# Performance work log

Hardware: AMD Instinct MI355X
Metric: run time of the kernel (lower is better)

Reference implementation:

```python
import jax, jax.numpy as jnp
import numpy as np

B, C, H, W = 256, 3, 224, 224
IMG_SIZE = 224
BRIGHT, CONTRAST, SAT, HUE = 0.2, 0.2, 0.2, 0.05
P_JITTER, P_CROP = 0.8, 0.5
SCALE_MIN, SCALE_MAX = 0.85, 1.0


def _blend(a, b, ratio):
    # torchvision _blend with float bound 1.0
    return jnp.clip(ratio * a + (1.0 - ratio) * b, 0.0, 1.0)


def _grayscale(x):
    # x: [B,3,H,W] -> [B,H,W]
    return 0.299 * x[:, 0] + 0.587 * x[:, 1] + 0.114 * x[:, 2]


def _adjust_hue(x, hue):
    # x: [B,3,H,W], hue: [B,1,1] offset in [-0.5,0.5]
    r, g, b = x[:, 0], x[:, 1], x[:, 2]
    maxc = jnp.maximum(jnp.maximum(r, g), b)
    minc = jnp.minimum(jnp.minimum(r, g), b)
    v = maxc
    cr = maxc - minc
    eqc = cr == 0.0
    s = cr / jnp.where(eqc, 1.0, maxc)
    crd = jnp.where(eqc, 1.0, cr)
    rc = (maxc - r) / crd
    gc = (maxc - g) / crd
    bc = (maxc - b) / crd
    h = ((maxc == r) * (bc - gc)
         + ((maxc == g) & (maxc != r)) * (2.0 + rc - bc)
         + ((maxc != g) & (maxc != r)) * (4.0 + gc - rc))
    h = jnp.mod(h / 6.0 + 1.0, 1.0)
    h = jnp.mod(h + hue, 1.0)
    # hsv -> rgb
    h6 = h * 6.0
    i = jnp.floor(h6)
    f = h6 - i
    i = i.astype(jnp.int32) % 6
    p = v * (1.0 - s)
    q = v * (1.0 - s * f)
    t = v * (1.0 - s * (1.0 - f))
    m = [(i == k) for k in range(6)]
    r2 = m[0] * v + m[1] * q + m[2] * p + m[3] * p + m[4] * t + m[5] * v
    g2 = m[0] * t + m[1] * v + m[2] * v + m[3] * q + m[4] * p + m[5] * p
    b2 = m[0] * p + m[1] * p + m[2] * t + m[3] * v + m[4] * v + m[5] * q
    return jnp.stack([r2, g2, b2], axis=1)


def _crop_resize_one(im, top, left, ch, cw):
    # im: [C,H,W]; bilinear resize of crop box to IMG_SIZE x IMG_SIZE
    Hh, Ww = im.shape[1], im.shape[2]
    S = IMG_SIZE
    ys = jnp.clip(top + (jnp.arange(S) + 0.5) * ch / S - 0.5, 0.0, Hh - 1.0)
    xs = jnp.clip(left + (jnp.arange(S) + 0.5) * cw / S - 0.5, 0.0, Ww - 1.0)
    y0 = jnp.floor(ys); x0 = jnp.floor(xs)
    wy = (ys - y0)[None, :, None]  # [1,S,1]
    wx = (xs - x0)[None, None, :]  # [1,1,S]
    y0i = y0.astype(jnp.int32); y1i = jnp.minimum(y0i + 1, Hh - 1)
    x0i = x0.astype(jnp.int32); x1i = jnp.minimum(x0i + 1, Ww - 1)
    g = lambda yi, xi: im[:, yi[:, None], xi[None, :]]  # [C,S,S]
    row0 = (1.0 - wx) * g(y0i, x0i) + wx * g(y0i, x1i)
    row1 = (1.0 - wx) * g(y1i, x0i) + wx * g(y1i, x1i)
    return (1.0 - wy) * row0 + wy * row1


def _forward(img, u_jitter, u_bright, u_contrast, u_sat, u_hue, u_crop, u_scale, u_top, u_left):
    # --- color jitter (fixed op order: brightness, contrast, saturation, hue) ---
    bf = (1.0 + (2.0 * u_bright - 1.0) * BRIGHT)[:, None, None, None]
    cf = (1.0 + (2.0 * u_contrast - 1.0) * CONTRAST)[:, None, None, None]
    sf = (1.0 + (2.0 * u_sat - 1.0) * SAT)[:, None, None, None]
    hf = ((2.0 * u_hue - 1.0) * HUE)[:, None, None]
    x = _blend(img, jnp.zeros_like(img), bf)                      # brightness
    mean_gray = _grayscale(x).mean(axis=(-2, -1))[:, None, None, None]
    x = _blend(x, mean_gray, cf)                                  # contrast
    x = _blend(x, _grayscale(x)[:, None], sf)                     # saturation
    x = _adjust_hue(x, hf)                                        # hue
    x = jnp.clip(x, 0.0, 1.0)
    jitter_on = (u_jitter < P_JITTER)[:, None, None, None]
    img = jnp.where(jitter_on, x, img)
    # --- random crop + resize back to IMG_SIZE ---
    Hh, Ww = img.shape[2], img.shape[3]
    scale = SCALE_MIN + (SCALE_MAX - SCALE_MIN) * u_scale
    ch = jnp.floor(Hh * scale)
    cw = jnp.floor(Ww * scale)
    top = jnp.clip(jnp.floor(u_top * (Hh - ch + 1.0)), 0.0, Hh - ch)
    left = jnp.clip(jnp.floor(u_left * (Ww - cw + 1.0)), 0.0, Ww - cw)
    resized = jax.vmap(_crop_resize_one)(img, top, left, ch, cw)
    crop_on = (u_crop < P_CROP)[:, None, None, None]
    return jnp.where(crop_on, resized, img)


def setup_inputs() -> dict:
    key = jax.random.key(0)
    ks = jax.random.split(key, 10)
    names = ['u_jitter', 'u_bright', 'u_contrast', 'u_sat', 'u_hue',
             'u_crop', 'u_scale', 'u_top', 'u_left']
    inp = {'img': jax.random.uniform(ks[0], (B, C, H, W), dtype=jnp.float32)}
    for i, n in enumerate(names):
        inp[n] = jax.random.uniform(ks[i + 1], (B,), dtype=jnp.float32)
    return inp


def reference(img, u_jitter, u_bright, u_contrast, u_sat, u_hue, u_crop, u_scale, u_top, u_left):
    return _forward(img, u_jitter, u_bright, u_contrast, u_sat, u_hue,
                    u_crop, u_scale, u_top, u_left)
```

## Files before the change

### kernel.cpp

```cpp
#include <hip/hip_runtime.h>


static constexpr int   kB      = 256;
static constexpr int   kHW     = 224;
static constexpr int   kHW4    = kHW / 4;
static constexpr int   kNPix   = kHW * kHW;
static constexpr int   kPlane  = kNPix;
static constexpr int   kPlane4 = kNPix / 4;
static constexpr int   kRows   = 8;
static constexpr int   kSrcRows = kRows + 1;
static constexpr int   kParts  = 8;
static constexpr int   kQuadsPerPart = kPlane4 / kParts;

__device__ __forceinline__ float clamp01(float x) {
    return fminf(fmaxf(x, 0.0f), 1.0f);
}

__device__ __forceinline__ float fast_rcp(float x) {
#if __has_builtin(__builtin_amdgcn_rcpf)
    return __builtin_amdgcn_rcpf(x);
#else
    return 1.0f / x;
#endif
}

struct Px { float r, g, b; };

__device__ __forceinline__ Px jitter_px(Px p, float bf, float cf, float sf,
                                        float hf, float oc) {
    float r = clamp01(bf * p.r);
    float g = clamp01(bf * p.g);
    float b = clamp01(bf * p.b);
    r = clamp01(cf * r + oc);
    g = clamp01(cf * g + oc);
    b = clamp01(cf * b + oc);
    float gray = 0.299f * r + 0.587f * g + 0.114f * b;
    float os = (1.0f - sf) * gray;
    r = clamp01(sf * r + os);
    g = clamp01(sf * g + os);
    b = clamp01(sf * b + os);
    float maxc = fmaxf(fmaxf(r, g), b);
    float minc = fminf(fminf(r, g), b);
    float v  = maxc;
    float cr = maxc - minc;
    bool  eqc = (cr == 0.0f);
    float s   = eqc ? 0.0f : cr * fast_rcp(maxc);
    float inv = eqc ? 1.0f : fast_rcp(cr);
    float rc = (maxc - r) * inv;
    float gc = (maxc - g) * inv;
    float bc = (maxc - b) * inv;
    float h = (maxc == r) ? (bc - gc)
            : (maxc == g) ? (2.0f + rc - bc)
                          : (4.0f + gc - rc);
    h = h * 0.16666667f + 1.0f;
    h = h - floorf(h);
    h = h + hf;
    h = h - floorf(h);
    float h6 = h * 6.0f;
    float fi = floorf(h6);
    float f  = h6 - fi;
    int   i  = ((int)fi) % 6;
    float pp = v * (1.0f - s);
    float qq = v * (1.0f - s * f);
    float tt = v * (1.0f - s * (1.0f - f));
    float r2 = (i == 1) ? qq : ((i == 2) || (i == 3)) ? pp : (i == 4) ? tt : v;
    float g2 = (i == 0) ? tt : ((i == 1) || (i == 2)) ? v  : (i == 3) ? qq : pp;
    float b2 = ((i == 0) || (i == 1)) ? pp : (i == 2) ? tt : (i == 5) ? qq : v;
    Px o;
    o.r = clamp01(r2);
    o.g = clamp01(g2);
    o.b = clamp01(b2);
    return o;
}

__device__ __forceinline__ void jitter_quad(float4& r4, float4& g4, float4& b4,
                                            float bf, float cf, float sf,
                                            float hf, float oc) {
    Px a0 = jitter_px({r4.x, g4.x, b4.x}, bf, cf, sf, hf, oc);
    Px a1 = jitter_px({r4.y, g4.y, b4.y}, bf, cf, sf, hf, oc);
    Px a2 = jitter_px({r4.z, g4.z, b4.z}, bf, cf, sf, hf, oc);
    Px a3 = jitter_px({r4.w, g4.w, b4.w}, bf, cf, sf, hf, oc);
    r4 = {a0.r, a1.r, a2.r, a3.r};
    g4 = {a0.g, a1.g, a2.g, a3.g};
    b4 = {a0.b, a1.b, a2.b, a3.b};
}

__global__ __launch_bounds__(256)
void gray_mean_kernel(const float* __restrict__ img,
                      const float* __restrict__ u_jitter,
                      const float* __restrict__ u_bright,
                      float* __restrict__ gray_part)
{
    const int b    = blockIdx.y;
    const int part = blockIdx.x;
    if (u_jitter[b] >= 0.8f) return;
    const float bf = 1.0f + (2.0f * u_bright[b] - 1.0f) * 0.2f;
    const float4* pr = (const float4*)(img + (size_t)b * 3 * kPlane)
                     + part * kQuadsPerPart;
    const float4* pg = pr + kPlane4;
    const float4* pb = pr + 2 * kPlane4;
    float acc = 0.0f;
    for (int i = threadIdx.x; i < kQuadsPerPart; i += 256) {
        float4 r = pr[i], g = pg[i], bl = pb[i];
        acc += 0.299f * clamp01(bf * r.x) + 0.587f * clamp01(bf * g.x) + 0.114f * clamp01(bf * bl.x);
        acc += 0.299f * clamp01(bf * r.y) + 0.587f * clamp01(bf * g.y) + 0.114f * clamp01(bf * bl.y);
        acc += 0.299f * clamp01(bf * r.z) + 0.587f * clamp01(bf * g.z) + 0.114f * clamp01(bf * bl.z);
        acc += 0.299f * clamp01(bf * r.w) + 0.587f * clamp01(bf * g.w) + 0.114f * clamp01(bf * bl.w);
    }
#pragma unroll
    for (int off = 32; off > 0; off >>= 1)
        acc += __shfl_down(acc, off);
    __shared__ float red[4];
    const int lane = threadIdx.x & 63;
    const int w    = threadIdx.x >> 6;
    if (lane == 0) red[w] = acc;
    __syncthreads();
    if (threadIdx.x == 0)
        gray_part[b * kParts + part] = red[0] + red[1] + red[2] + red[3];
}

__global__ __launch_bounds__(256)
void aug_main_kernel(const float* __restrict__ img,
                     const float* __restrict__ u_jitter,
                     const float* __restrict__ u_bright,
                     const float* __restrict__ u_contrast,
                     const float* __restrict__ u_sat,
                     const float* __restrict__ u_hue,
                     const float* __restrict__ u_crop,
                     const float* __restrict__ u_scale,
                     const float* __restrict__ u_top,
                     const float* __restrict__ u_left,
                     const float* __restrict__ gray_part,
                     float* __restrict__ out)
{
    const int b   = blockIdx.y;
    const int oy0 = blockIdx.x * kRows;
    const int t   = threadIdx.x;

    const bool jitter_on = u_jitter[b] < 0.8f;
    const bool crop_on   = u_crop[b]   < 0.5f;

    float bf = 1.0f, cf = 1.0f, sf = 1.0f, hf = 0.0f, oc = 0.0f;
    if (jitter_on) {
        bf = 1.0f + (2.0f * u_bright[b]   - 1.0f) * 0.2f;
        cf = 1.0f + (2.0f * u_contrast[b] - 1.0f) * 0.2f;
        sf = 1.0f + (2.0f * u_sat[b]      - 1.0f) * 0.2f;
        hf = (2.0f * u_hue[b] - 1.0f) * 0.05f;
        float s = 0.0f;
#pragma unroll
        for (int k = 0; k < kParts; ++k) s += gray_part[b * kParts + k];
        const float mg = s * (1.0f / (float)kNPix);
        oc = (1.0f - cf) * mg;
    }

    const float*  base  = img + (size_t)b * 3 * kPlane;
    float*        obase = out + (size_t)b * 3 * kPlane;
    const float4* p4    = (const float4*)base;
    float4*       o4    = (float4*)obase;

    if (!crop_on) {
        for (int q = t; q < kRows * kHW4; q += 256) {
            const int f4 = oy0 * kHW4 + q;
            float4 r4 = p4[f4];
            float4 g4 = p4[f4 + kPlane4];
            float4 b4 = p4[f4 + 2 * kPlane4];
            if (jitter_on) jitter_quad(r4, g4, b4, bf, cf, sf, hf, oc);
            o4[f4]               = r4;
            o4[f4 + kPlane4]     = g4;
            o4[f4 + 2 * kPlane4] = b4;
        }
        return;
    }

    float ch, top, left;
    {
#pragma clang fp contract(off)
        float scale = 0.85f + 0.15f * u_scale[b];
        ch = floorf(224.0f * scale);
        float rem = (224.0f - ch) + 1.0f;
        top  = fminf(fmaxf(floorf(u_top[b]  * rem), 0.0f), 224.0f - ch);
        left = fminf(fmaxf(floorf(u_left[b] * rem), 0.0f), 224.0f - ch);
    }

    int ybase;
    {
#pragma clang fp contract(off)
        float fy0 = top + ((float)oy0 + 0.5f) * ch / 224.0f - 0.5f;
        fy0 = fminf(fmaxf(fy0, 0.0f), 223.0f);
        ybase = (int)floorf(fy0);
    }
    ybase = min(ybase, kHW - kSrcRows);

    __shared__ float sm[3][kSrcRows * kHW];

    for (int q = t; q < kSrcRows * kHW4; q += 256) {
        const int r  = q / kHW4;
        const int xq = q - r * kHW4;
        const int gi = (ybase + r) * kHW4 + xq;
        float4 r4 = p4[gi];
        float4 g4 = p4[gi + kPlane4];
        float4 b4 = p4[gi + 2 * kPlane4];
        if (jitter_on) jitter_quad(r4, g4, b4, bf, cf, sf, hf, oc);
        const int so = r * kHW + xq * 4;
        *(float4*)&sm[0][so] = r4;
        *(float4*)&sm[1][so] = g4;
        *(float4*)&sm[2][so] = b4;
    }
    __syncthreads();

    for (int p = t; p < kRows * kHW; p += 256) {
        const int dy = p / kHW;
        const int ox = p - dy * kHW;
        const int oy = oy0 + dy;
        float fy;
        {
#pragma clang fp contract(off)
            fy = top + ((float)oy + 0.5f) * ch / 224.0f - 0.5f;
        }
        fy = fminf(fmaxf(fy, 0.0f), 223.0f);
        const float y0f = floorf(fy);
        const float wy  = fy - y0f;
        const int   y0  = (int)y0f;
        const int   y1  = min(y0 + 1, kHW - 1);
        const int   r0  = (y0 - ybase) * kHW;
        const int   r1  = (y1 - ybase) * kHW;

        float fx;
        {
#pragma clang fp contract(off)
            fx = left + ((float)ox + 0.5f) * ch / 224.0f - 0.5f;
        }
        fx = fminf(fmaxf(fx, 0.0f), 223.0f);
        const float x0f = floorf(fx);
        const float wx  = fx - x0f;
        const int   x0  = (int)x0f;
        const int   x1  = min(x0 + 1, kHW - 1);

        const int oo = oy * kHW + ox;
#pragma unroll
        for (int c = 0; c < 3; ++c) {
            const float v00 = sm[c][r0 + x0];
            const float v01 = sm[c][r0 + x1];
            const float v10 = sm[c][r1 + x0];
            const float v11 = sm[c][r1 + x1];
            const float a0 = (1.0f - wx) * v00 + wx * v01;
            const float a1 = (1.0f - wx) * v10 + wx * v11;
            obase[c * kPlane + oo] = (1.0f - wy) * a0 + wy * a1;
        }
    }
}

extern "C" void kernel_launch(void* const* d_in, const int* in_sizes, int n_in,
                              void* d_out, int out_size, void* d_ws, size_t ws_size,
                              hipStream_t stream) {
    const float* img = (const float*)d_in[0];
    const float* uj  = (const float*)d_in[1];
    const float* ub  = (const float*)d_in[2];
    const float* uc  = (const float*)d_in[3];
    const float* us  = (const float*)d_in[4];
    const float* uh  = (const float*)d_in[5];
    const float* ucr = (const float*)d_in[6];
    const float* usc = (const float*)d_in[7];
    const float* ut  = (const float*)d_in[8];
    const float* ul  = (const float*)d_in[9];
    float* gray_part = (float*)d_ws;
    float* out       = (float*)d_out;

    gray_mean_kernel<<<dim3(kParts, kB), 256, 0, stream>>>(img, uj, ub, gray_part);

    dim3 gridB(kHW / kRows, kB, 1);
    aug_main_kernel<<<gridB, 256, 0, stream>>>(img, uj, ub, uc, us, uh,
                                               ucr, usc, ut, ul, gray_part, out);
}
```

Before: 301.9 us.

## Fuse gray-mean reduction into main kernel via atomic work-claiming

Replaces the separate gray-mean reduction kernel with a fused kernel. Blocks of the same image claim reduction parts through atomic CAS, publish partial sums, and spin-wait until all parts for that image are done before applying jitter. A small reset kernel zeroes the claim and counter state on every launch. The aim is to overlap the reduction with the main pass and let the image data be reused from L2. In exchange it risks spin-waiting and relies on forward progress across blocks, since a waiting block depends on claimed parts finishing.

```diff
diff --git a/kernel.cpp b/kernel.cpp
--- a/kernel.cpp
+++ b/kernel.cpp
@@ -11,6 +11,8 @@
 static constexpr int   kSrcRows = kRows + 1;
 static constexpr int   kParts  = 8;
 static constexpr int   kQuadsPerPart = kPlane4 / kParts;
+static constexpr int   kNState = kB * kParts;
+static constexpr int   kNReset = kNState + kB;
 
 __device__ __forceinline__ float clamp01(float x) {
     return fminf(fmaxf(x, 0.0f), 1.0f);
@@ -86,52 +88,27 @@
 }
 
 __global__ __launch_bounds__(256)
-void gray_mean_kernel(const float* __restrict__ img,
+void reset_ws_kernel(int* __restrict__ ws)
+{
+    const int i = blockIdx.x * 256 + threadIdx.x;
+    if (i < kNReset) ws[i] = 0;
+}
+
+__global__ __launch_bounds__(256)
+void aug_fused_kernel(const float* __restrict__ img,
                       const float* __restrict__ u_jitter,
                       const float* __restrict__ u_bright,
-                      float* __restrict__ gray_part)
-{
-    const int b    = blockIdx.y;
-    const int part = blockIdx.x;
-    if (u_jitter[b] >= 0.8f) return;
-    const float bf = 1.0f + (2.0f * u_bright[b] - 1.0f) * 0.2f;
-    const float4* pr = (const float4*)(img + (size_t)b * 3 * kPlane)
-                     + part * kQuadsPerPart;
-    const float4* pg = pr + kPlane4;
-    const float4* pb = pr + 2 * kPlane4;
-    float acc = 0.0f;
-    for (int i = threadIdx.x; i < kQuadsPerPart; i += 256) {
-        float4 r = pr[i], g = pg[i], bl = pb[i];
-        acc += 0.299f * clamp01(bf * r.x) + 0.587f * clamp01(bf * g.x) + 0.114f * clamp01(bf * bl.x);
-        acc += 0.299f * clamp01(bf * r.y) + 0.587f * clamp01(bf * g.y) + 0.114f * clamp01(bf * bl.y);
-        acc += 0.299f * clamp01(bf * r.z) + 0.587f * clamp01(bf * g.z) + 0.114f * clamp01(bf * bl.z);
-        acc += 0.299f * clamp01(bf * r.w) + 0.587f * clamp01(bf * g.w) + 0.114f * clamp01(bf * bl.w);
-    }
-#pragma unroll
-    for (int off = 32; off > 0; off >>= 1)
-        acc += __shfl_down(acc, off);
-    __shared__ float red[4];
-    const int lane = threadIdx.x & 63;
-    const int w    = threadIdx.x >> 6;
-    if (lane == 0) red[w] = acc;
-    __syncthreads();
-    if (threadIdx.x == 0)
-        gray_part[b * kParts + part] = red[0] + red[1] + red[2] + red[3];
-}
-
-__global__ __launch_bounds__(256)
-void aug_main_kernel(const float* __restrict__ img,
-                     const float* __restrict__ u_jitter,
-                     const float* __restrict__ u_bright,
-                     const float* __restrict__ u_contrast,
-                     const float* __restrict__ u_sat,
-                     const float* __restrict__ u_hue,
-                     const float* __restrict__ u_crop,
-                     const float* __restrict__ u_scale,
-                     const float* __restrict__ u_top,
-                     const float* __restrict__ u_left,
-                     const float* __restrict__ gray_part,
-                     float* __restrict__ out)
+                      const float* __restrict__ u_contrast,
+                      const float* __restrict__ u_sat,
+                      const float* __restrict__ u_hue,
+                      const float* __restrict__ u_crop,
+                      const float* __restrict__ u_scale,
+                      const float* __restrict__ u_top,
+                      const float* __restrict__ u_left,
+                      int*   __restrict__ state,
+                      int*   __restrict__ done,
+                      float* __restrict__ gpart,
+                      float* __restrict__ out)
 {
     const int b   = blockIdx.y;
     const int oy0 = blockIdx.x * kRows;
@@ -139,6 +116,16 @@
 
     const bool jitter_on = u_jitter[b] < 0.8f;
     const bool crop_on   = u_crop[b]   < 0.5f;
+
+    const float*  base  = img + (size_t)b * 3 * kPlane;
+    float*        obase = out + (size_t)b * 3 * kPlane;
+    const float4* p4    = (const float4*)base;
+    float4*       o4    = (float4*)obase;
+
+    __shared__ float sm[3][kSrcRows * kHW];
+    __shared__ float red[4];
+    __shared__ int   s_claim;
+    __shared__ float s_mean;
 
     float bf = 1.0f, cf = 1.0f, sf = 1.0f, hf = 0.0f, oc = 0.0f;
     if (jitter_on) {
@@ -146,17 +133,65 @@
         cf = 1.0f + (2.0f * u_contrast[b] - 1.0f) * 0.2f;
         sf = 1.0f + (2.0f * u_sat[b]      - 1.0f) * 0.2f;
         hf = (2.0f * u_hue[b] - 1.0f) * 0.05f;
-        float s = 0.0f;
+
+        for (int p = 0; p < kParts; ++p) {
+            if (t == 0) {
+                int c = 0;
+                if (__hip_atomic_load(&done[b], __ATOMIC_RELAXED,
+                                      __HIP_MEMORY_SCOPE_AGENT) < kParts &&
+                    __hip_atomic_load(&state[b * kParts + p], __ATOMIC_RELAXED,
+                                      __HIP_MEMORY_SCOPE_AGENT) == 0) {
+                    c = (atomicCAS(&state[b * kParts + p], 0, 1) == 0);
+                }
+                s_claim = c;
+            }
+            __syncthreads();
+            const int cl = s_claim;
+            __syncthreads();
+            if (!cl) continue;
+
+            const float4* pr = p4 + p * kQuadsPerPart;
+            const float4* pg = pr + kPlane4;
+            const float4* pb = pr + 2 * kPlane4;
+            float acc = 0.0f;
+            for (int i = t; i < kQuadsPerPart; i += 256) {
+                float4 r = pr[i], g = pg[i], bl = pb[i];
+                acc += 0.299f * clamp01(bf * r.x) + 0.587f * clamp01(bf * g.x) + 0.114f * clamp01(bf * bl.x);
+                acc += 0.299f * clamp01(bf * r.y) + 0.587f * clamp01(bf * g.y) + 0.114f * clamp01(bf * bl.y);
+                acc += 0.299f * clamp01(bf * r.z) + 0.587f * clamp01(bf * g.z) + 0.114f * clamp01(bf * bl.z);
+                acc += 0.299f * clamp01(bf * r.w) + 0.587f * clamp01(bf * g.w) + 0.114f * clamp01(bf * bl.w);
+            }
 #pragma unroll
-        for (int k = 0; k < kParts; ++k) s += gray_part[b * kParts + k];
-        const float mg = s * (1.0f / (float)kNPix);
-        oc = (1.0f - cf) * mg;
-    }
-
-    const float*  base  = img + (size_t)b * 3 * kPlane;
-    float*        obase = out + (size_t)b * 3 * kPlane;
-    const float4* p4    = (const float4*)base;
-    float4*       o4    = (float4*)obase;
+            for (int off = 32; off > 0; off >>= 1)
+                acc += __shfl_down(acc, off);
+            const int lane = t & 63;
+            const int w    = t >> 6;
+            if (lane == 0) red[w] = acc;
+            __syncthreads();
+            if (t == 0) {
+                const float s = red[0] + red[1] + red[2] + red[3];
+                __hip_atomic_store(&gpart[b * kParts + p], s,
+                                   __ATOMIC_RELAXED, __HIP_MEMORY_SCOPE_AGENT);
+                __hip_atomic_fetch_add(&done[b], 1,
+                                       __ATOMIC_RELEASE, __HIP_MEMORY_SCOPE_AGENT);
+            }
+            __syncthreads();
+        }
+
+        if (t == 0) {
+            while (__hip_atomic_load(&done[b], __ATOMIC_ACQUIRE,
+                                     __HIP_MEMORY_SCOPE_AGENT) < kParts)
+                __builtin_amdgcn_s_sleep(8);
+            float s = 0.0f;
+#pragma unroll
+            for (int k = 0; k < kParts; ++k)
+                s += __hip_atomic_load(&gpart[b * kParts + k],
+                                       __ATOMIC_RELAXED, __HIP_MEMORY_SCOPE_AGENT);
+            s_mean = s * (1.0f / (float)kNPix);
+        }
+        __syncthreads();
+        oc = (1.0f - cf) * s_mean;
+    }
 
     if (!crop_on) {
         for (int q = t; q < kRows * kHW4; q += 256) {
@@ -190,8 +225,6 @@
         ybase = (int)floorf(fy0);
     }
     ybase = min(ybase, kHW - kSrcRows);
-
-    __shared__ float sm[3][kSrcRows * kHW];
 
     for (int q = t; q < kSrcRows * kHW4; q += 256) {
         const int r  = q / kHW4;
@@ -263,12 +296,16 @@
     const float* usc = (const float*)d_in[7];
     const float* ut  = (const float*)d_in[8];
     const float* ul  = (const float*)d_in[9];
-    float* gray_part = (float*)d_ws;
-    float* out       = (float*)d_out;
-
-    gray_mean_kernel<<<dim3(kParts, kB), 256, 0, stream>>>(img, uj, ub, gray_part);
+
+    int*   state = (int*)d_ws;
+    int*   done  = state + kNState;
+    float* gpart = (float*)(done + kB);
+    float* out   = (float*)d_out;
+
+    reset_ws_kernel<<<dim3((kNReset + 255) / 256), 256, 0, stream>>>(state);
 
     dim3 gridB(kHW / kRows, kB, 1);
-    aug_main_kernel<<<gridB, 256, 0, stream>>>(img, uj, ub, uc, us, uh,
-                                               ucr, usc, ut, ul, gray_part, out);
-}
+    aug_fused_kernel<<<gridB, 256, 0, stream>>>(img, uj, ub, uc, us, uh,
+                                                ucr, usc, ut, ul,
+                                                state, done, gpart, out);
+}
```

Measured after the change: 682.6 us. 126% more time.
